# Kernel optimization log

Measured on AMD Instinct MI355X. Metric: run time of the kernel, lower is better.

Reference implementation:

```python
import jax, jax.numpy as jnp
import numpy as np
import math

D_MODEL, N_HEADS, D_FF = 1024, 16, 4096
HEAD_DIM = D_MODEL // N_HEADS
BATCH, SEQ = 2, 2048
POPE_BASE = 10000.0
LN_EPS = 1e-5


def setup_inputs() -> dict:
    key = jax.random.key(0)
    ks = jax.random.split(key, 20)
    s = 0.02
    inp = {
        "x": jax.random.normal(ks[0], (BATCH, SEQ, D_MODEL), dtype=jnp.float32),
        "positions": jnp.arange(SEQ, dtype=jnp.int64) if jax.config.jax_enable_x64 else jnp.arange(SEQ, dtype=jnp.int32),
        "Wq": jax.random.normal(ks[1], (D_MODEL, D_MODEL), jnp.float32) * s,
        "bq": jnp.zeros((D_MODEL,), jnp.float32),
        "Wk": jax.random.normal(ks[2], (D_MODEL, D_MODEL), jnp.float32) * s,
        "bk": jnp.zeros((D_MODEL,), jnp.float32),
        "Wv": jax.random.normal(ks[3], (D_MODEL, D_MODEL), jnp.float32) * s,
        "bv": jnp.zeros((D_MODEL,), jnp.float32),
        "Wo": jax.random.normal(ks[4], (D_MODEL, D_MODEL), jnp.float32) * s,
        "bo": jnp.zeros((D_MODEL,), jnp.float32),
        "phase_bias": jax.random.uniform(ks[5], (N_HEADS, HEAD_DIM), jnp.float32,
                                          minval=-2.0 * math.pi, maxval=0.0),
        "freqs": (1.0 / POPE_BASE ** (jnp.arange(HEAD_DIM, dtype=jnp.float32) / HEAD_DIM)),
        "W1": jax.random.normal(ks[6], (D_MODEL, D_FF), jnp.float32) * s,
        "b1": jnp.zeros((D_FF,), jnp.float32),
        "W2": jax.random.normal(ks[7], (D_FF, D_MODEL), jnp.float32) * s,
        "b2": jnp.zeros((D_MODEL,), jnp.float32),
        "g1": jnp.ones((D_MODEL,), jnp.float32),
        "beta1": jnp.zeros((D_MODEL,), jnp.float32),
        "g2": jnp.ones((D_MODEL,), jnp.float32),
        "beta2": jnp.zeros((D_MODEL,), jnp.float32),
    }
    return inp


def _layernorm(x, g, b):
    mu = jnp.mean(x, axis=-1, keepdims=True)
    var = jnp.mean((x - mu) ** 2, axis=-1, keepdims=True)
    return (x - mu) * jax.lax.rsqrt(var + LN_EPS) * g + b


def reference(x, positions, Wq, bq, Wk, bk, Wv, bv, Wo, bo, phase_bias, freqs,
              W1, b1, W2, b2, g1, beta1, g2, beta2):
    B, S, D = x.shape
    H, hd = N_HEADS, HEAD_DIM

    def split_heads(y):  # (B,S,D) -> (B,H,S,hd)
        return y.reshape(B, S, H, hd).transpose(0, 2, 1, 3)

    q = split_heads(x @ Wq + bq)
    k = split_heads(x @ Wk + bk)
    v = split_heads(x @ Wv + bv)

    # --- PoPE: magnitudes via softplus, phases from positions + learned bias ---
    mu_q = jax.nn.softplus(q)
    mu_k = jax.nn.softplus(k)
    pos_phases = positions[:, None].astype(jnp.float32) * freqs[None, :]        # (S,hd)
    phases = pos_phases[None, None, :, :] + phase_bias[None, :, None, :]        # (1,H,S,hd)
    cosp, sinp = jnp.cos(phases), jnp.sin(phases)
    q_pope = jnp.concatenate([mu_q * cosp, mu_q * sinp], axis=-1)               # (B,H,S,2hd)
    k_pope = jnp.concatenate([mu_k * cosp, mu_k * sinp], axis=-1)

    # --- manual causal attention with softmax1 ---
    scale = 1.0 / math.sqrt(2 * hd)  # q.shape[-1] == 2*head_dim under PoPE
    scores = jnp.einsum("bhsd,bhtd->bhst", q_pope, k_pope) * scale
    causal = jnp.triu(jnp.ones((S, S), dtype=bool), k=1)
    scores = jnp.where(causal[None, None], -jnp.inf, scores)
    m = jnp.max(scores, axis=-1, keepdims=True)
    e = jnp.exp(scores - m)
    attn_w = e / (1.0 + jnp.sum(e, axis=-1, keepdims=True))  # softmax1 (as written in source)
    attn = jnp.einsum("bhst,bhtd->bhsd", attn_w, v)

    attn = attn.transpose(0, 2, 1, 3).reshape(B, S, D) @ Wo + bo
    x = _layernorm(x + attn, g1, beta1)
    ff = jax.nn.relu(x @ W1 + b1) @ W2 + b2
    x = _layernorm(x + ff, g2, beta2)
    return x
```

## Files before the change

kernel.cpp:

```cpp
#include <hip/hip_runtime.h>
#include <hip/hip_bf16.h>
#include <math.h>

#define B_   2
#define S_   2048
#define D_   1024
#define H_   16
#define HD_  64
#define DFF_ 4096
#define M_   (B_*S_)
#define SCALE_ 0.08838834764831845f

typedef __attribute__((ext_vector_type(8))) short bf16x8;
typedef __attribute__((ext_vector_type(4))) float f32x4;

#define MFMA16(a,b,c) __builtin_amdgcn_mfma_f32_16x16x32_bf16((a),(b),(c),0,0,0)

__device__ __forceinline__ unsigned short f2b(float f) {
    union { float f; unsigned u; } v; v.f = f;
    return (unsigned short)((v.u + 0x7FFFu + ((v.u >> 16) & 1u)) >> 16);
}
__device__ __forceinline__ float b2f(unsigned short s) {
    union { unsigned u; float f; } v; v.u = ((unsigned)s) << 16;
    return v.f;
}
__device__ __forceinline__ float softplus_f(float x) {
    return fmaxf(x, 0.f) + log1pf(__expf(-fabsf(x)));
}
__device__ __forceinline__ void g2l16(const void* g, void* l) {
    __builtin_amdgcn_global_load_lds(
        (const __attribute__((address_space(1))) unsigned int*)g,
        (__attribute__((address_space(3))) unsigned int*)l, 16, 0, 0);
}

__global__ __launch_bounds__(256) void conv_bf16_kernel(
    const float* __restrict__ in, unsigned short* __restrict__ out)
{
    int i = blockIdx.x * 256 + threadIdx.x;
    out[i] = f2b(in[i]);
}

__global__ __launch_bounds__(256) void wtrans_kernel(
    const float* __restrict__ W, unsigned short* __restrict__ WT, int K, int N)
{
    __shared__ float tile[32][33];
    const int n0 = blockIdx.x * 32, k0 = blockIdx.y * 32;
    const int tx = threadIdx.x & 31, ty = threadIdx.x >> 5;
    #pragma unroll
    for (int i = 0; i < 4; i++)
        tile[ty + 8*i][tx] = W[(size_t)(k0 + ty + 8*i) * N + n0 + tx];
    __syncthreads();
    #pragma unroll
    for (int i = 0; i < 4; i++)
        WT[(size_t)(n0 + ty + 8*i) * K + k0 + tx] = f2b(tile[tx][ty + 8*i]);
}

__global__ __launch_bounds__(256) void bcat_kernel(
    const float* __restrict__ a, const float* __restrict__ b,
    const float* __restrict__ c, float* __restrict__ o)
{
    int i = blockIdx.x * 256 + threadIdx.x;
    o[i] = (i < 1024) ? a[i] : (i < 2048 ? b[i - 1024] : c[i - 2048]);
}

__global__ __launch_bounds__(256) void gemm_bf16_kernel(
    const unsigned short* __restrict__ A,
    const unsigned short* __restrict__ WT,
    const float* __restrict__ bias,
    float* __restrict__ outF, unsigned short* __restrict__ outB,
    int M, int Kslice, int lda, int N, int relu)
{
    __shared__ unsigned short As[128 * 64];
    __shared__ unsigned short Bs[128 * 64];

    const int tid = threadIdx.x;
    const int w = tid >> 6, lane = tid & 63;
    const int quad = lane >> 4, l16 = lane & 15;
    const size_t m0 = (size_t)blockIdx.y * 128, n0 = (size_t)blockIdx.x * 128;
    const int wm = (w >> 1) * 64, wn = (w & 1) * 64;
    const int koff = blockIdx.z * Kslice;

    const int srow = lane >> 3;
    const int sc   = ((lane & 7) ^ srow) * 8;
    const unsigned short* ga = A  + (m0 + w * 32 + srow) * (size_t)lda + koff + sc;
    const unsigned short* gb = WT + (n0 + w * 32 + srow) * (size_t)lda + koff + sc;
    const size_t rows8 = (size_t)8 * lda;

    f32x4 acc[4][4] = {};

    for (int k0 = 0; k0 < Kslice; k0 += 64) {
        #pragma unroll
        for (int j = 0; j < 4; j++)
            g2l16(ga + j * rows8 + k0, &As[(w * 32 + j * 8) * 64]);
        #pragma unroll
        for (int j = 0; j < 4; j++)
            g2l16(gb + j * rows8 + k0, &Bs[(w * 32 + j * 8) * 64]);
        __syncthreads();

        #pragma unroll
        for (int kk = 0; kk < 2; kk++) {
            bf16x8 af[4], bfr[4];
            #pragma unroll
            for (int t = 0; t < 4; t++) {
                const int slot = ((kk * 4 + quad) ^ (l16 & 7)) * 8;
                af[t]  = *(const bf16x8*)&As[(wm + t * 16 + l16) * 64 + slot];
                bfr[t] = *(const bf16x8*)&Bs[(wn + t * 16 + l16) * 64 + slot];
            }
            #pragma unroll
            for (int mt = 0; mt < 4; mt++)
                #pragma unroll
                for (int nt = 0; nt < 4; nt++)
                    acc[mt][nt] = MFMA16(af[mt], bfr[nt], acc[mt][nt]);
        }
        __syncthreads();
    }

    float bv[4];
    #pragma unroll
    for (int nt = 0; nt < 4; nt++)
        bv[nt] = (blockIdx.z == 0) ? bias[n0 + wn + nt * 16 + l16] : 0.f;

    float* outFz = outF ? outF + (size_t)blockIdx.z * M * N : nullptr;

    #pragma unroll
    for (int mt = 0; mt < 4; mt++) {
        #pragma unroll
        for (int nt = 0; nt < 4; nt++) {
            const size_t n = n0 + wn + nt * 16 + l16;
            #pragma unroll
            for (int r = 0; r < 4; r++) {
                const size_t m = m0 + wm + mt * 16 + quad * 4 + r;
                float val = acc[mt][nt][r] + bv[nt];
                if (relu) val = fmaxf(val, 0.f);
                const size_t idx = m * N + n;
                if (outFz) outFz[idx] = val;
                if (outB) outB[idx] = f2b(val);
            }
        }
    }
}

__global__ __launch_bounds__(256) void pope_kernel(
    const unsigned short* __restrict__ qkv,
    const float* __restrict__ phase_bias, const float* __restrict__ freqs,
    unsigned short* __restrict__ qp, unsigned short* __restrict__ kp)
{
    int idx = blockIdx.x * 256 + threadIdx.x;
    int d = idx & 63;
    int s = (idx >> 6) & (S_ - 1);
    int h = (idx >> 17) & (H_ - 1);
    int b = idx >> 21;

    size_t src = (size_t)(b * S_ + s) * 3072 + h * HD_ + d;
    float muq = softplus_f(b2f(qkv[src])) * SCALE_;
    float muk = softplus_f(b2f(qkv[src + 1024]));

    float ph = (float)s * freqs[d] + phase_bias[h * HD_ + d];
    float sn, cs;
    sincosf(ph, &sn, &cs);

    size_t o = ((size_t)(b * H_ + h) * S_ + s) * 128 + d;
    qp[o]      = f2b(muq * cs);
    qp[o + 64] = f2b(muq * sn);
    kp[o]      = f2b(muk * cs);
    kp[o + 64] = f2b(muk * sn);
}

__global__ __launch_bounds__(256) void vtrans_kernel(
    const unsigned short* __restrict__ qkv, unsigned short* __restrict__ vt)
{
    __shared__ unsigned short tile[64][72];
    const int bh = blockIdx.y, b = bh >> 4, h = bh & 15;
    const int s0 = blockIdx.x * 64;
    const int tid = threadIdx.x;
    #pragma unroll
    for (int i = 0; i < 16; i++) {
        int idx = i * 256 + tid;
        int s = idx >> 6, d = idx & 63;
        tile[s][d] = qkv[(size_t)(b * S_ + s0 + s) * 3072 + 2048 + h * HD_ + d];
    }
    __syncthreads();
    #pragma unroll
    for (int i = 0; i < 16; i++) {
        int idx = i * 256 + tid;
        int d = idx >> 6, s = idx & 63;
        vt[((size_t)bh * 64 + d) * S_ + s0 + s] = tile[s][d];
    }
}

__global__ __launch_bounds__(512) void attn_mfma_kernel(
    const unsigned short* __restrict__ qp,
    const unsigned short* __restrict__ kp,
    const unsigned short* __restrict__ vt,
    unsigned short* __restrict__ ao)
{
    __shared__ unsigned short kt_lds[2][64][128];
    __shared__ unsigned short vt_lds[2][64][64];
    __shared__ unsigned short p_lds[8][16][72];

    const int tid = threadIdx.x;
    const int w = tid >> 6, lane = tid & 63;
    const int quad = lane >> 4, l16 = lane & 15;
    const int bh = blockIdx.y, b = bh >> 4, h = bh & 15;

    const int krow = lane >> 4, kslot = lane & 15;
    const int vrow = lane >> 3, vslot = lane & 7;

    #pragma unroll 1
    for (int part = 0; part < 2; part++) {
        const int a = part == 0 ? (int)blockIdx.x : 15 - (int)blockIdx.x;
        const int q0b = a * 128;
        const int q0 = q0b + w * 16;

        const unsigned short* qbase = qp + ((size_t)bh * S_ + q0 + l16) * 128 + quad * 8;
        bf16x8 qa[4];
        #pragma unroll
        for (int kc = 0; kc < 4; kc++) qa[kc] = *(const bf16x8*)(qbase + kc * 32);

        f32x4 o[4] = {};
        float ms = -1e30f, ls = 0.f;

        const int ntiles = (q0b >> 6) + 2;

        __syncthreads();
        #pragma unroll
        for (int j = 0; j < 2; j++) {
            const int r = w * 8 + j * 4 + krow;
            const int c = kslot ^ (r & 15);
            g2l16(kp + ((size_t)bh * S_ + r) * 128 + c * 8, &kt_lds[0][w * 8 + j * 4][0]);
        }
        {
            const int d = w * 8 + vrow;
            const int c = vslot ^ (d & 7);
            g2l16(vt + ((size_t)bh * 64 + d) * S_ + c * 8, &vt_lds[0][w * 8][0]);
        }

        for (int ti = 0; ti < ntiles; ti++) {
            const int t0 = ti * 64;
            __syncthreads();
            if (ti + 1 < ntiles) {
                const int nb = (ti + 1) & 1, nt0 = t0 + 64;
                #pragma unroll
                for (int j = 0; j < 2; j++) {
                    const int r = w * 8 + j * 4 + krow;
                    const int c = kslot ^ (r & 15);
                    g2l16(kp + ((size_t)bh * S_ + nt0 + r) * 128 + c * 8,
                          &kt_lds[nb][w * 8 + j * 4][0]);
                }
                {
                    const int d = w * 8 + vrow;
                    const int c = vslot ^ (d & 7);
                    g2l16(vt + ((size_t)bh * 64 + d) * S_ + nt0 + c * 8,
                          &vt_lds[nb][w * 8][0]);
                }
            }
            const int buf = ti & 1;

            if (t0 <= q0 + 15) {
                f32x4 sf[4];
                #pragma unroll
                for (int kg = 0; kg < 4; kg++) {
                    f32x4 s = {0, 0, 0, 0};
                    const int row = kg * 16 + l16;
                    #pragma unroll
                    for (int kc = 0; kc < 4; kc++) {
                        const int slot = (kc * 4 + quad) ^ l16;
                        s = MFMA16(*(const bf16x8*)&kt_lds[buf][row][slot * 8], qa[kc], s);
                    }
                    sf[kg] = s;
                }

                const int qrow = q0 + l16;
                #pragma unroll
                for (int kg = 0; kg < 4; kg++) {
                    const int kbase = t0 + kg * 16 + quad * 4;
                    ushort4 pk;
                    unsigned short* pkp = (unsigned short*)&pk;
                    float esum = 0.f;
                    #pragma unroll
                    for (int r = 0; r < 4; r++) {
                        const float v = (kbase + r <= qrow) ? sf[kg][r] : -1e30f;
                        ms = fmaxf(ms, v);
                        const float e = __expf(v);
                        esum += e;
                        pkp[r] = f2b(e);
                    }
                    ls += esum;
                    *(ushort4*)&p_lds[w][l16][kg * 16 + quad * 4] = pk;
                }
                asm volatile("s_waitcnt lgkmcnt(0)" ::: "memory");
                bf16x8 pa0 = *(const bf16x8*)&p_lds[w][l16][quad * 8];
                bf16x8 pa1 = *(const bf16x8*)&p_lds[w][l16][quad * 8 + 32];

                #pragma unroll
                for (int dg = 0; dg < 4; dg++) {
                    const int row = dg * 16 + l16;
                    const int s0_ = quad ^ (l16 & 7);
                    const int s1_ = (quad + 4) ^ (l16 & 7);
                    o[dg] = MFMA16(pa0, *(const bf16x8*)&vt_lds[buf][row][s0_ * 8], o[dg]);
                    o[dg] = MFMA16(pa1, *(const bf16x8*)&vt_lds[buf][row][s1_ * 8], o[dg]);
                }
            }
        }

        float mv = ms, lv = ls;
        mv = fmaxf(mv, __shfl_xor(mv, 16, 64)); lv += __shfl_xor(lv, 16, 64);
        mv = fmaxf(mv, __shfl_xor(mv, 32, 64)); lv += __shfl_xor(lv, 32, 64);
        const float inv = 1.f / (__expf(mv) + lv);

        #pragma unroll
        for (int r = 0; r < 4; r++) {
            const float ir = __shfl(inv, quad * 4 + r, 64);
            const int row = q0 + quad * 4 + r;
            const size_t base = (size_t)(b * S_ + row) * D_ + h * HD_ + l16;
            ao[base]      = f2b(o[0][r] * ir);
            ao[base + 16] = f2b(o[1][r] * ir);
            ao[base + 32] = f2b(o[2][r] * ir);
            ao[base + 48] = f2b(o[3][r] * ir);
        }
    }
}

__global__ __launch_bounds__(256) void ln_kernel(
    const float* __restrict__ ya, const float* __restrict__ yb,
    const float* __restrict__ res,
    const float* __restrict__ g, const float* __restrict__ beta,
    float* __restrict__ out, unsigned short* __restrict__ outB)
{
    const int row = blockIdx.x;
    const int tid = threadIdx.x;
    const float* yr = ya + (size_t)row * D_;
    const float* y2 = yb ? yb + (size_t)row * D_ : nullptr;
    const float* rr = res + (size_t)row * D_;

    float t[4];
    float sum = 0.f, sumsq = 0.f;
    #pragma unroll
    for (int i = 0; i < 4; i++) {
        int c = tid + 256 * i;
        t[i] = yr[c] + rr[c] + (y2 ? y2[c] : 0.f);
        sum += t[i]; sumsq += t[i] * t[i];
    }
    #pragma unroll
    for (int off = 32; off >= 1; off >>= 1) {
        sum   += __shfl_xor(sum,   off, 64);
        sumsq += __shfl_xor(sumsq, off, 64);
    }
    __shared__ float rs_[4], rq_[4];
    int w = tid >> 6, lane = tid & 63;
    if (lane == 0) { rs_[w] = sum; rq_[w] = sumsq; }
    __syncthreads();
    float tot  = rs_[0] + rs_[1] + rs_[2] + rs_[3];
    float totq = rq_[0] + rq_[1] + rq_[2] + rq_[3];
    float mu   = tot  * (1.f / D_);
    float var  = totq * (1.f / D_) - mu * mu;
    float rstd = rsqrtf(var + 1e-5f);

    float* orow = out + (size_t)row * D_;
    #pragma unroll
    for (int i = 0; i < 4; i++) {
        int c = tid + 256 * i;
        float val = (t[i] - mu) * rstd * g[c] + beta[c];
        orow[c] = val;
        if (outB) outB[(size_t)row * D_ + c] = f2b(val);
    }
}

extern "C" void kernel_launch(void* const* d_in, const int* in_sizes, int n_in,
                              void* d_out, int out_size, void* d_ws, size_t ws_size,
                              hipStream_t stream)
{
    const float* x   = (const float*)d_in[0];
    const float* Wq  = (const float*)d_in[2];
    const float* bq  = (const float*)d_in[3];
    const float* Wk  = (const float*)d_in[4];
    const float* bk  = (const float*)d_in[5];
    const float* Wv  = (const float*)d_in[6];
    const float* bv  = (const float*)d_in[7];
    const float* Wo  = (const float*)d_in[8];
    const float* bo  = (const float*)d_in[9];
    const float* phase_bias = (const float*)d_in[10];
    const float* freqs = (const float*)d_in[11];
    const float* W1  = (const float*)d_in[12];
    const float* b1  = (const float*)d_in[13];
    const float* W2  = (const float*)d_in[14];
    const float* b2  = (const float*)d_in[15];
    const float* g1  = (const float*)d_in[16];
    const float* be1 = (const float*)d_in[17];
    const float* g2  = (const float*)d_in[18];
    const float* be2 = (const float*)d_in[19];
    float* out = (float*)d_out;

    char* base = (char*)d_ws;
    const size_t MiB = 1024 * 1024;
    unsigned short* WqkvT = (unsigned short*)(base);
    unsigned short* WoT   = (unsigned short*)(base + 6  * MiB);
    unsigned short* W1T   = (unsigned short*)(base + 8  * MiB);
    unsigned short* W2T   = (unsigned short*)(base + 16 * MiB);
    float*          bqkv  = (float*)(base + 24 * MiB);
    unsigned short* xb    = (unsigned short*)(base + 25 * MiB);
    unsigned short* qkvb  = (unsigned short*)(base + 33 * MiB);
    unsigned short* qpb   = (unsigned short*)(base + 57 * MiB);
    unsigned short* kpb   = (unsigned short*)(base + 73 * MiB);
    unsigned short* vtb   = (unsigned short*)(base + 89 * MiB);
    float*          po    = (float*)(base + 89 * MiB);
    float*          x1    = (float*)(base + 121 * MiB);
    unsigned short* aob   = xb;
    unsigned short* x1b   = xb;
    unsigned short* hb    = qkvb;
    float*          fo    = po;

    dim3 blk(256);

    conv_bf16_kernel<<<dim3(M_ * D_ / 256), blk, 0, stream>>>(x, xb);
    wtrans_kernel<<<dim3(32, 32), blk, 0, stream>>>(Wq, WqkvT, D_, D_);
    wtrans_kernel<<<dim3(32, 32), blk, 0, stream>>>(Wk, WqkvT + (size_t)1024 * 1024, D_, D_);
    wtrans_kernel<<<dim3(32, 32), blk, 0, stream>>>(Wv, WqkvT + (size_t)2048 * 1024, D_, D_);
    wtrans_kernel<<<dim3(32, 32), blk, 0, stream>>>(Wo, WoT, D_, D_);
    wtrans_kernel<<<dim3(DFF_ / 32, D_ / 32), blk, 0, stream>>>(W1, W1T, D_, DFF_);
    wtrans_kernel<<<dim3(D_ / 32, DFF_ / 32), blk, 0, stream>>>(W2, W2T, DFF_, D_);
    bcat_kernel<<<dim3(12), blk, 0, stream>>>(bq, bk, bv, bqkv);

    gemm_bf16_kernel<<<dim3(3072 / 128, M_ / 128, 1), blk, 0, stream>>>(
        xb, WqkvT, bqkv, nullptr, qkvb, M_, D_, D_, 3072, 0);

    pope_kernel<<<dim3(B_ * H_ * S_ * HD_ / 256), blk, 0, stream>>>(
        qkvb, phase_bias, freqs, qpb, kpb);
    vtrans_kernel<<<dim3(S_ / 64, B_ * H_), blk, 0, stream>>>(qkvb, vtb);

    attn_mfma_kernel<<<dim3(8, B_ * H_), dim3(512), 0, stream>>>(qpb, kpb, vtb, aob);

    gemm_bf16_kernel<<<dim3(D_ / 128, M_ / 128, 2), blk, 0, stream>>>(
        aob, WoT, bo, po, nullptr, M_, D_ / 2, D_, D_, 0);
    ln_kernel<<<dim3(M_), blk, 0, stream>>>(po, po + (size_t)M_ * D_, x, g1, be1, x1, x1b);

    gemm_bf16_kernel<<<dim3(DFF_ / 128, M_ / 128, 1), blk, 0, stream>>>(
        x1b, W1T, b1, nullptr, hb, M_, D_, D_, DFF_, 1);
    gemm_bf16_kernel<<<dim3(D_ / 128, M_ / 128, 2), blk, 0, stream>>>(
        hb, W2T, b2, fo, nullptr, M_, DFF_ / 2, DFF_, D_, 0);
    ln_kernel<<<dim3(M_), blk, 0, stream>>>(fo, fo + (size_t)M_ * D_, x1, g2, be2, out, nullptr);
}
```

Before: 426.9 us.

## Split paired attention query tiles across grid z and simplify softmax packing

```diff
diff --git a/kernel.cpp b/kernel.cpp
--- a/kernel.cpp
+++ b/kernel.cpp
@@ -23,6 +23,10 @@
 __device__ __forceinline__ float b2f(unsigned short s) {
     union { unsigned u; float f; } v; v.u = ((unsigned)s) << 16;
     return v.f;
+}
+__device__ __forceinline__ unsigned pk2bf(float a, float b) {
+    union { float f; unsigned u; } ua, ub; ua.f = a; ub.f = b;
+    return __builtin_amdgcn_perm(ub.u, ua.u, 0x07060302u);
 }
 __device__ __forceinline__ float softplus_f(float x) {
     return fmaxf(x, 0.f) + log1pf(__expf(-fabsf(x)));
@@ -188,7 +192,7 @@
     }
 }
 
-__global__ __launch_bounds__(512) void attn_mfma_kernel(
+__global__ __launch_bounds__(512, 4) void attn_mfma_kernel(
     const unsigned short* __restrict__ qp,
     const unsigned short* __restrict__ kp,
     const unsigned short* __restrict__ vt,
@@ -203,121 +207,110 @@
     const int quad = lane >> 4, l16 = lane & 15;
     const int bh = blockIdx.y, b = bh >> 4, h = bh & 15;
 
+    const int a = (blockIdx.z == 0) ? 15 - (int)blockIdx.x : (int)blockIdx.x;
+    const int q0b = a * 128;
+    const int q0 = q0b + w * 16;
+
+    const unsigned short* qbase = qp + ((size_t)bh * S_ + q0 + l16) * 128 + quad * 8;
+    bf16x8 qa[4];
+    #pragma unroll
+    for (int kc = 0; kc < 4; kc++) qa[kc] = *(const bf16x8*)(qbase + kc * 32);
+
     const int krow = lane >> 4, kslot = lane & 15;
     const int vrow = lane >> 3, vslot = lane & 7;
-
-    #pragma unroll 1
-    for (int part = 0; part < 2; part++) {
-        const int a = part == 0 ? (int)blockIdx.x : 15 - (int)blockIdx.x;
-        const int q0b = a * 128;
-        const int q0 = q0b + w * 16;
-
-        const unsigned short* qbase = qp + ((size_t)bh * S_ + q0 + l16) * 128 + quad * 8;
-        bf16x8 qa[4];
-        #pragma unroll
-        for (int kc = 0; kc < 4; kc++) qa[kc] = *(const bf16x8*)(qbase + kc * 32);
-
-        f32x4 o[4] = {};
-        float ms = -1e30f, ls = 0.f;
-
-        const int ntiles = (q0b >> 6) + 2;
-
+    const int kr0 = w * 8 + krow,     kc0 = kslot ^ (kr0 & 15);
+    const int kr1 = w * 8 + 4 + krow, kc1 = kslot ^ (kr1 & 15);
+    const int vd  = w * 8 + vrow,     vc  = vslot ^ (vd & 7);
+    const unsigned short* kg0 = kp + ((size_t)bh * S_ + kr0) * 128 + kc0 * 8;
+    const unsigned short* kg1 = kp + ((size_t)bh * S_ + kr1) * 128 + kc1 * 8;
+    const unsigned short* vg0 = vt + ((size_t)bh * 64 + vd) * S_ + vc * 8;
+
+    f32x4 o[4] = {};
+    float ms = -1e30f, ls = 0.f;
+
+    const int ntiles = 2 * a + 2;
+
+    g2l16(kg0, &kt_lds[0][w * 8][0]);
+    g2l16(kg1, &kt_lds[0][w * 8 + 4][0]);
+    g2l16(vg0, &vt_lds[0][w * 8][0]);
+
+    for (int ti = 0; ti < ntiles; ti++) {
+        const int t0 = ti * 64;
         __syncthreads();
-        #pragma unroll
-        for (int j = 0; j < 2; j++) {
-            const int r = w * 8 + j * 4 + krow;
-            const int c = kslot ^ (r & 15);
-            g2l16(kp + ((size_t)bh * S_ + r) * 128 + c * 8, &kt_lds[0][w * 8 + j * 4][0]);
+        if (ti + 1 < ntiles) {
+            const int nb = (ti + 1) & 1;
+            const size_t ko = (size_t)(ti + 1) * (64 * 128);
+            const size_t vo = (size_t)(ti + 1) * 64;
+            g2l16(kg0 + ko, &kt_lds[nb][w * 8][0]);
+            g2l16(kg1 + ko, &kt_lds[nb][w * 8 + 4][0]);
+            g2l16(vg0 + vo, &vt_lds[nb][w * 8][0]);
         }
-        {
-            const int d = w * 8 + vrow;
-            const int c = vslot ^ (d & 7);
-            g2l16(vt + ((size_t)bh * 64 + d) * S_ + c * 8, &vt_lds[0][w * 8][0]);
-        }
-
-        for (int ti = 0; ti < ntiles; ti++) {
-            const int t0 = ti * 64;
-            __syncthreads();
-            if (ti + 1 < ntiles) {
-                const int nb = (ti + 1) & 1, nt0 = t0 + 64;
+        const int buf = ti & 1;
+
+        if (t0 <= q0 + 15) {
+            f32x4 sf[4];
+            #pragma unroll
+            for (int kg = 0; kg < 4; kg++) {
+                f32x4 s = {0, 0, 0, 0};
+                const int row = kg * 16 + l16;
                 #pragma unroll
-                for (int j = 0; j < 2; j++) {
-                    const int r = w * 8 + j * 4 + krow;
-                    const int c = kslot ^ (r & 15);
-                    g2l16(kp + ((size_t)bh * S_ + nt0 + r) * 128 + c * 8,
-                          &kt_lds[nb][w * 8 + j * 4][0]);
+                for (int kc = 0; kc < 4; kc++) {
+                    const int slot = (kc * 4 + quad) ^ l16;
+                    s = MFMA16(*(const bf16x8*)&kt_lds[buf][row][slot * 8], qa[kc], s);
                 }
-                {
-                    const int d = w * 8 + vrow;
-                    const int c = vslot ^ (d & 7);
-                    g2l16(vt + ((size_t)bh * 64 + d) * S_ + nt0 + c * 8,
-                          &vt_lds[nb][w * 8][0]);
+                sf[kg] = s;
+            }
+
+            const int qrow = q0 + l16;
+            const bool dmask = (t0 + 63 > q0);
+            #pragma unroll
+            for (int kg = 0; kg < 4; kg++) {
+                const int kbase = t0 + kg * 16 + quad * 4;
+                float v0 = sf[kg][0], v1 = sf[kg][1], v2 = sf[kg][2], v3 = sf[kg][3];
+                if (dmask) {
+                    v0 = (kbase     <= qrow) ? v0 : -1e30f;
+                    v1 = (kbase + 1 <= qrow) ? v1 : -1e30f;
+                    v2 = (kbase + 2 <= qrow) ? v2 : -1e30f;
+                    v3 = (kbase + 3 <= qrow) ? v3 : -1e30f;
                 }
+                ms = fmaxf(ms, fmaxf(fmaxf(v0, v1), fmaxf(v2, v3)));
+                const float e0 = __expf(v0), e1 = __expf(v1);
+                const float e2 = __expf(v2), e3 = __expf(v3);
+                ls += (e0 + e1) + (e2 + e3);
+                uint2 pk;
+                pk.x = pk2bf(e0, e1);
+                pk.y = pk2bf(e2, e3);
+                *(uint2*)&p_lds[w][l16][kg * 16 + quad * 4] = pk;
             }
-            const int buf = ti & 1;
-
-            if (t0 <= q0 + 15) {
-                f32x4 sf[4];
-                #pragma unroll
-                for (int kg = 0; kg < 4; kg++) {
-                    f32x4 s = {0, 0, 0, 0};
-                    const int row = kg * 16 + l16;
-                    #pragma unroll
-                    for (int kc = 0; kc < 4; kc++) {
-                        const int slot = (kc * 4 + quad) ^ l16;
-                        s = MFMA16(*(const bf16x8*)&kt_lds[buf][row][slot * 8], qa[kc], s);
-                    }
-                    sf[kg] = s;
-                }
-
-                const int qrow = q0 + l16;
-                #pragma unroll
-                for (int kg = 0; kg < 4; kg++) {
-                    const int kbase = t0 + kg * 16 + quad * 4;
-                    ushort4 pk;
-                    unsigned short* pkp = (unsigned short*)&pk;
-                    float esum = 0.f;
-                    #pragma unroll
-                    for (int r = 0; r < 4; r++) {
-                        const float v = (kbase + r <= qrow) ? sf[kg][r] : -1e30f;
-                        ms = fmaxf(ms, v);
-                        const float e = __expf(v);
-                        esum += e;
-                        pkp[r] = f2b(e);
-                    }
-                    ls += esum;
-                    *(ushort4*)&p_lds[w][l16][kg * 16 + quad * 4] = pk;
-                }
-                asm volatile("s_waitcnt lgkmcnt(0)" ::: "memory");
-                bf16x8 pa0 = *(const bf16x8*)&p_lds[w][l16][quad * 8];
-                bf16x8 pa1 = *(const bf16x8*)&p_lds[w][l16][quad * 8 + 32];
-
-                #pragma unroll
-                for (int dg = 0; dg < 4; dg++) {
-                    const int row = dg * 16 + l16;
-                    const int s0_ = quad ^ (l16 & 7);
-                    const int s1_ = (quad + 4) ^ (l16 & 7);
-                    o[dg] = MFMA16(pa0, *(const bf16x8*)&vt_lds[buf][row][s0_ * 8], o[dg]);
-                    o[dg] = MFMA16(pa1, *(const bf16x8*)&vt_lds[buf][row][s1_ * 8], o[dg]);
-                }
+            asm volatile("s_waitcnt lgkmcnt(0)" ::: "memory");
+            bf16x8 pa0 = *(const bf16x8*)&p_lds[w][l16][quad * 8];
+            bf16x8 pa1 = *(const bf16x8*)&p_lds[w][l16][quad * 8 + 32];
+
+            #pragma unroll
+            for (int dg = 0; dg < 4; dg++) {
+                const int row = dg * 16 + l16;
+                const int s0_ = quad ^ (l16 & 7);
+                const int s1_ = (quad + 4) ^ (l16 & 7);
+                o[dg] = MFMA16(pa0, *(const bf16x8*)&vt_lds[buf][row][s0_ * 8], o[dg]);
+                o[dg] = MFMA16(pa1, *(const bf16x8*)&vt_lds[buf][row][s1_ * 8], o[dg]);
             }
         }
-
-        float mv = ms, lv = ls;
-        mv = fmaxf(mv, __shfl_xor(mv, 16, 64)); lv += __shfl_xor(lv, 16, 64);
-        mv = fmaxf(mv, __shfl_xor(mv, 32, 64)); lv += __shfl_xor(lv, 32, 64);
-        const float inv = 1.f / (__expf(mv) + lv);
-
-        #pragma unroll
-        for (int r = 0; r < 4; r++) {
-            const float ir = __shfl(inv, quad * 4 + r, 64);
-            const int row = q0 + quad * 4 + r;
-            const size_t base = (size_t)(b * S_ + row) * D_ + h * HD_ + l16;
-            ao[base]      = f2b(o[0][r] * ir);
-            ao[base + 16] = f2b(o[1][r] * ir);
-            ao[base + 32] = f2b(o[2][r] * ir);
-            ao[base + 48] = f2b(o[3][r] * ir);
-        }
+    }
+
+    float mv = ms, lv = ls;
+    mv = fmaxf(mv, __shfl_xor(mv, 16, 64)); lv += __shfl_xor(lv, 16, 64);
+    mv = fmaxf(mv, __shfl_xor(mv, 32, 64)); lv += __shfl_xor(lv, 32, 64);
+    const float inv = 1.f / (__expf(mv) + lv);
+
+    #pragma unroll
+    for (int r = 0; r < 4; r++) {
+        const float ir = __shfl(inv, quad * 4 + r, 64);
+        const int row = q0 + quad * 4 + r;
+        const size_t base = (size_t)(b * S_ + row) * D_ + h * HD_ + l16;
+        ao[base]      = f2b(o[0][r] * ir);
+        ao[base + 16] = f2b(o[1][r] * ir);
+        ao[base + 32] = f2b(o[2][r] * ir);
+        ao[base + 48] = f2b(o[3][r] * ir);
     }
 }
 
@@ -428,7 +421,7 @@
         qkvb, phase_bias, freqs, qpb, kpb);
     vtrans_kernel<<<dim3(S_ / 64, B_ * H_), blk, 0, stream>>>(qkvb, vtb);
 
-    attn_mfma_kernel<<<dim3(8, B_ * H_), dim3(512), 0, stream>>>(qpb, kpb, vtb, aob);
+    attn_mfma_kernel<<<dim3(8, B_ * H_, 2), dim3(512), 0, stream>>>(qpb, kpb, vtb, aob);
 
     gemm_bf16_kernel<<<dim3(D_ / 128, M_ / 128, 2), blk, 0, stream>>>(
         aob, WoT, bo, po, nullptr, M_, D_ / 2, D_, D_, 0);
```

Measured after the change: 417.2 us. 2.3% less time.
